# Kernel optimization log

Measured on AMD Instinct MI355X. Metric: run time of the kernel, lower is better.

The kernel has to match this reference:

```python
import jax, jax.numpy as jnp
import numpy as np
import math

D_MODEL = 1024
N_HEADS = 16
B, T = 4, 2048


def setup_inputs() -> dict:
    key = jax.random.key(0)
    ks = jax.random.split(key, 10)
    s = 1.0 / math.sqrt(D_MODEL)
    x = jax.random.normal(ks[0], (B, T, D_MODEL), dtype=jnp.float32)
    # causal mask, broadcastable over batch and heads; 0 -> masked
    mask = jnp.tril(jnp.ones((T, T), dtype=jnp.int32))[None, None, :, :]
    w_q = jax.random.normal(ks[1], (D_MODEL, D_MODEL), dtype=jnp.float32) * s
    b_q = jnp.zeros((D_MODEL,), dtype=jnp.float32)
    w_k = jax.random.normal(ks[2], (D_MODEL, D_MODEL), dtype=jnp.float32) * s
    b_k = jnp.zeros((D_MODEL,), dtype=jnp.float32)
    w_v = jax.random.normal(ks[3], (D_MODEL, D_MODEL), dtype=jnp.float32) * s
    b_v = jnp.zeros((D_MODEL,), dtype=jnp.float32)
    w_o = jax.random.normal(ks[4], (D_MODEL, D_MODEL), dtype=jnp.float32) * s
    b_o = jnp.zeros((D_MODEL,), dtype=jnp.float32)
    return {"x": x, "mask": mask, "w_q": w_q, "b_q": b_q, "w_k": w_k,
            "b_k": b_k, "w_v": w_v, "b_v": b_v, "w_o": w_o, "b_o": b_o}


def reference(x, mask, w_q, b_q, w_k, b_k, w_v, b_v, w_o, b_o):
    Bx, Tx, C = x.shape
    H = N_HEADS
    d_k = C // H
    def split_heads(y):  # [B,T,C] -> [B,H,T,d_k]
        return y.reshape(Bx, Tx, H, d_k).transpose(0, 2, 1, 3)
    Q = split_heads(x @ w_q + b_q)
    K = split_heads(x @ w_k + b_k)
    V = split_heads(x @ w_v + b_v)
    scores = jnp.einsum('bhqd,bhkd->bhqk', Q, K) / math.sqrt(d_k)
    scores = jnp.where(mask == 0, jnp.float32(-1e9), scores)
    attn = jax.nn.softmax(scores, axis=-1)
    out = jnp.einsum('bhqk,bhkd->bhqd', attn, V)
    out = out.transpose(0, 2, 1, 3).reshape(Bx, Tx, C)
    return out @ w_o + b_o
```

## Files before the change

### kernel.cpp

```cpp
#include <hip/hip_runtime.h>
#include <stdint.h>

#define D_MODEL 1024
#define NH      16
#define BB      4
#define TT      2048
#define MROWS   (BB * TT)

typedef __attribute__((ext_vector_type(8))) short bf16x8;
typedef __attribute__((ext_vector_type(4))) short bf16x4;
typedef __attribute__((ext_vector_type(4))) float f32x4;

__device__ __forceinline__ unsigned short f2bf(float f) {
    union { float f; unsigned int u; } v; v.f = f;
    unsigned int r = v.u + 0x7fffu + ((v.u >> 16) & 1u);
    return (unsigned short)(r >> 16);
}

__device__ __forceinline__ unsigned short f2bf_fast(float f) {
    union { float f; unsigned int u; } v; v.f = f;
    return (unsigned short)((v.u + 0x8000u) >> 16);
}

__device__ __forceinline__ f32x4 mfma_16x16x16_bf16(bf16x4 a, bf16x4 b, f32x4 c) {
    asm("v_mfma_f32_16x16x16_bf16 %0, %1, %2, %0" : "+v"(c) : "v"(a), "v"(b));
    return c;
}

__device__ __forceinline__ void gload_lds16(const unsigned short* g, unsigned short* l) {
    __builtin_amdgcn_global_load_lds(
        (const __attribute__((address_space(1))) void*)g,
        (__attribute__((address_space(3))) void*)l,
        16, 0, 0);
}

__global__ void convert_x_kernel(const float* __restrict__ x, unsigned short* __restrict__ xb) {
    int i = blockIdx.x * 256 + threadIdx.x;
    float4 v = ((const float4*)x)[i];
    ushort4 o;
    o.x = f2bf(v.x); o.y = f2bf(v.y); o.z = f2bf(v.z); o.w = f2bf(v.w);
    ((ushort4*)xb)[i] = o;
}

__global__ void transpose_w_kernel(const float* __restrict__ wq, const float* __restrict__ wk,
                                   const float* __restrict__ wv, const float* __restrict__ wo,
                                   unsigned short* tq, unsigned short* tk,
                                   unsigned short* tv, unsigned short* to_) {
    const float* src; unsigned short* dst;
    switch (blockIdx.z) {
        case 0:  src = wq; dst = tq; break;
        case 1:  src = wk; dst = tk; break;
        case 2:  src = wv; dst = tv; break;
        default: src = wo; dst = to_; break;
    }
    __shared__ float tile[32][33];
    int tx = threadIdx.x & 31, ty = threadIdx.x >> 5;
    int k0 = blockIdx.y * 32, n0 = blockIdx.x * 32;
    #pragma unroll
    for (int i = 0; i < 4; ++i)
        tile[ty + i * 8][tx] = src[(k0 + ty + i * 8) * D_MODEL + n0 + tx];
    __syncthreads();
    #pragma unroll
    for (int i = 0; i < 4; ++i)
        dst[(n0 + ty + i * 8) * D_MODEL + k0 + tx] = f2bf(tile[tx][ty + i * 8]);
}

__device__ __forceinline__ void gemm_mainloop(const unsigned short* __restrict__ A,
                                              const unsigned short* __restrict__ Bt,
                                              int m0, int n0,
                                              unsigned short* As, unsigned short* Bs,
                                              f32x4 acc[4][4]) {
    const int tid = threadIdx.x;
    const int lane = tid & 63, wave = tid >> 6;
    const int wm = (wave >> 1) * 64, wn = (wave & 1) * 64;
    const int l15 = lane & 15, quad = lane >> 4;
    const int rx7 = l15 & 7;
    const int srow = tid >> 3;
    const int scol = ((tid & 7) ^ (srow & 7)) * 8;
    const unsigned short* Ag = A + (size_t)(m0 + srow) * D_MODEL + scol;
    const unsigned short* Bg = Bt + (size_t)(n0 + srow) * D_MODEL + scol;
    unsigned short* AsW = As + wave * 512;
    unsigned short* BsW = Bs + wave * 512;
    for (int k0 = 0; k0 < D_MODEL; k0 += 64) {
        __syncthreads();
        #pragma unroll
        for (int p = 0; p < 4; ++p) {
            gload_lds16(Ag + k0 + (size_t)(32 * p) * D_MODEL, AsW + (32 * p) * 64);
            gload_lds16(Bg + k0 + (size_t)(32 * p) * D_MODEL, BsW + (32 * p) * 64);
        }
        __syncthreads();
        #pragma unroll
        for (int kk = 0; kk < 2; ++kk) {
            const int co = ((kk * 4 + quad) ^ rx7) * 8;
            bf16x8 af[4], bfr[4];
            #pragma unroll
            for (int mt = 0; mt < 4; ++mt)
                af[mt] = *(const bf16x8*)(As + (wm + mt * 16 + l15) * 64 + co);
            #pragma unroll
            for (int nt = 0; nt < 4; ++nt)
                bfr[nt] = *(const bf16x8*)(Bs + (wn + nt * 16 + l15) * 64 + co);
            #pragma unroll
            for (int mt = 0; mt < 4; ++mt)
                #pragma unroll
                for (int nt = 0; nt < 4; ++nt)
                    acc[mt][nt] = __builtin_amdgcn_mfma_f32_16x16x32_bf16(af[mt], bfr[nt], acc[mt][nt], 0, 0, 0);
        }
    }
}

__global__ __launch_bounds__(256, 2) void gemm_qkv_kernel(
        const unsigned short* __restrict__ Xb, const unsigned short* __restrict__ Wt,
        const float* __restrict__ bq, const float* __restrict__ bk, const float* __restrict__ bv,
        unsigned short* __restrict__ Qo, unsigned short* __restrict__ Ko,
        unsigned short* __restrict__ VTo) {
    __shared__ unsigned short S[18432];
    unsigned short* As = S;
    unsigned short* Bs = S + 8192;
    int m0 = blockIdx.y * 128, n0 = blockIdx.x * 128;
    f32x4 acc[4][4];
    #pragma unroll
    for (int mt = 0; mt < 4; ++mt)
        #pragma unroll
        for (int nt = 0; nt < 4; ++nt)
            acc[mt][nt] = (f32x4){0.f, 0.f, 0.f, 0.f};
    gemm_mainloop(Xb, Wt, m0, n0, As, Bs, acc);

    const int sel = n0 >> 10;
    const float* bias = (sel == 0) ? bq : (sel == 1) ? bk : bv;
    const float scale = (sel == 0) ? 0.125f * 1.44269504f : 1.f;
    const int tid = threadIdx.x, lane = tid & 63, wave = tid >> 6;
    const int wm = (wave >> 1) * 64, wn = (wave & 1) * 64, l15 = lane & 15, quad = lane >> 4;
    if (sel < 2) {
        unsigned short* Out = (sel == 0) ? Qo : Ko;
        __syncthreads();
        unsigned short* R = S + (wn >> 6) * 9216;
        #pragma unroll
        for (int nt = 0; nt < 4; ++nt) {
            int ln = nt * 16 + l15;
            int col = (n0 + wn + nt * 16 + l15) & 1023;
            float bv_ = bias[col];
            #pragma unroll
            for (int mt = 0; mt < 4; ++mt)
                #pragma unroll
                for (int r = 0; r < 4; ++r) {
                    int lm = wm + mt * 16 + quad * 4 + r;
                    R[lm * 72 + ln] = f2bf((acc[mt][nt][r] + bv_) * scale);
                }
        }
        __syncthreads();
        int hh = tid >> 7, t = tid & 127;
        int h0 = (n0 & 1023) >> 6;
        int b = m0 >> 11, tb = m0 & 2047;
        unsigned short* gp = Out + (size_t)((b * NH + h0 + hh) * TT + tb + t) * 64;
        const unsigned short* lp = S + hh * 9216 + t * 72;
        #pragma unroll
        for (int j = 0; j < 8; ++j)
            *(uint4*)(gp + j * 8) = *(const uint4*)(lp + j * 8);
    } else {
        #pragma unroll
        for (int nt = 0; nt < 4; ++nt) {
            int col = (n0 + wn + nt * 16 + l15) & 1023;
            float bv_ = bias[col];
            int h = col >> 6, dd = col & 63;
            #pragma unroll
            for (int mt = 0; mt < 4; ++mt) {
                int gm0 = m0 + wm + mt * 16 + quad * 4;
                int b = gm0 >> 11, t0 = gm0 & 2047;
                ushort4 o;
                o.x = f2bf(acc[mt][nt][0] + bv_);
                o.y = f2bf(acc[mt][nt][1] + bv_);
                o.z = f2bf(acc[mt][nt][2] + bv_);
                o.w = f2bf(acc[mt][nt][3] + bv_);
                *(ushort4*)&VTo[(((size_t)(b * NH + h) * 16 + (t0 >> 7)) * 64 + dd) * 128 + (t0 & 127)] = o;
            }
        }
    }
}

__global__ __launch_bounds__(256, 2) void gemm_out_kernel(
        const unsigned short* __restrict__ Ob, const unsigned short* __restrict__ Wto,
        const float* __restrict__ bo, float* __restrict__ out) {
    __shared__ unsigned short As[128 * 64], Bs[128 * 64];
    int m0 = blockIdx.y * 128, n0 = blockIdx.x * 128;
    f32x4 acc[4][4];
    #pragma unroll
    for (int mt = 0; mt < 4; ++mt)
        #pragma unroll
        for (int nt = 0; nt < 4; ++nt)
            acc[mt][nt] = (f32x4){0.f, 0.f, 0.f, 0.f};
    gemm_mainloop(Ob, Wto, m0, n0, As, Bs, acc);
    const int tid = threadIdx.x, lane = tid & 63, wave = tid >> 6;
    const int wm = (wave >> 1) * 64, wn = (wave & 1) * 64, l15 = lane & 15, quad = lane >> 4;
    #pragma unroll
    for (int nt = 0; nt < 4; ++nt) {
        int gn = n0 + wn + nt * 16 + l15;
        float bv_ = bo[gn];
        #pragma unroll
        for (int mt = 0; mt < 4; ++mt) {
            #pragma unroll
            for (int r = 0; r < 4; ++r) {
                int gm = m0 + wm + mt * 16 + quad * 4 + r;
                out[(size_t)gm * D_MODEL + gn] = acc[mt][nt][r] + bv_;
            }
        }
    }
}

__global__ __launch_bounds__(256, 4) void flash_kernel(
        const unsigned short* __restrict__ Q, const unsigned short* __restrict__ K,
        const unsigned short* __restrict__ VT, unsigned short* __restrict__ O) {
    __shared__ unsigned short S[16384];
    unsigned short* Kd = S;
    unsigned short* Vd = S + 8192;
    const int n = blockIdx.x;
    const int bh = n & 63;
    const int qt = 15 - (n >> 6);
    const int q0 = qt * 128;
    const int tid = threadIdx.x, lane = tid & 63, wave = tid >> 6;
    const int l15 = lane & 15, quad = lane >> 4;
    const int mbase = wave * 32;
    const unsigned short* Qb = Q + (size_t)bh * (TT * 64) + (size_t)q0 * 64;
    const unsigned short* Kb = K + (size_t)bh * (TT * 64);
    const unsigned short* Vtb = VT + (size_t)bh * (16 * 8192);

    int koff[2], voff[2];
    #pragma unroll
    for (int p = 0; p < 2; ++p) {
        int c = p * 256 + tid;
        int r = c >> 3, s = c & 7;
        koff[p] = r * 64 + ((s ^ (r & 7)) * 8);
        voff[p] = r * 128 + ((s ^ (r & 7)) * 8);
    }
    auto fire = [&](int kt, int buf) {
        const unsigned short* Ksrc = Kb + kt * 4096;
        const unsigned short* Vsrc = Vtb + (kt >> 1) * 8192 + (kt & 1) * 64;
        #pragma unroll
        for (int p = 0; p < 2; ++p) {
            gload_lds16(Ksrc + koff[p], Kd + buf * 4096 + (p * 256 + wave * 64) * 8);
            gload_lds16(Vsrc + voff[p], Vd + buf * 4096 + (p * 256 + wave * 64) * 8);
        }
    };

    bf16x8 qf[2][2];
    #pragma unroll
    for (int mt = 0; mt < 2; ++mt)
        #pragma unroll
        for (int kk = 0; kk < 2; ++kk)
            qf[mt][kk] = *(const bf16x8*)(Qb + (size_t)(mbase + mt * 16 + l15) * 64 + kk * 32 + quad * 8);

    float l_full[2] = {0.f, 0.f};
    f32x4 acc[2][4];
    #pragma unroll
    for (int mt = 0; mt < 2; ++mt)
        #pragma unroll
        for (int nt = 0; nt < 4; ++nt) acc[mt][nt] = (f32x4){0.f, 0.f, 0.f, 0.f};

    fire(0, 0);

    const int nkt = 2 * qt + 2;
    for (int kt = 0; kt < nkt; ++kt) {
        const int p = kt & 1;
        __syncthreads();
        if (kt + 1 < nkt) fire(kt + 1, p ^ 1);
        if (kt * 64 > q0 + mbase + 31) continue;
        const unsigned short* Ksl = Kd + p * 4096;
        const unsigned short* Vsl = Vd + p * 4096;

        #pragma unroll 1
        for (int s4 = 0; s4 < 2; ++s4) {
            f32x4 sf[2][2];
            #pragma unroll
            for (int mt = 0; mt < 2; ++mt)
                #pragma unroll
                for (int ntl = 0; ntl < 2; ++ntl) sf[mt][ntl] = (f32x4){0.f, 0.f, 0.f, 0.f};
            __builtin_amdgcn_s_setprio(1);
            #pragma unroll
            for (int kk = 0; kk < 2; ++kk)
                #pragma unroll
                for (int ntl = 0; ntl < 2; ++ntl) {
                    int row = s4 * 32 + ntl * 16 + l15;
                    bf16x8 kf = *(const bf16x8*)&Ksl[row * 64 + (((kk * 4 + quad) ^ (row & 7)) * 8)];
                    #pragma unroll
                    for (int mt = 0; mt < 2; ++mt)
                        sf[mt][ntl] = __builtin_amdgcn_mfma_f32_16x16x32_bf16(kf, qf[mt][kk], sf[mt][ntl], 0, 0, 0);
                }
            __builtin_amdgcn_s_setprio(0);
            if (kt >= 2 * qt) {
                const int kofs = (kt - 2 * qt) * 64;
                #pragma unroll
                for (int mt = 0; mt < 2; ++mt) {
                    int qi = mbase + mt * 16 + l15;
                    #pragma unroll
                    for (int ntl = 0; ntl < 2; ++ntl)
                        #pragma unroll
                        for (int r = 0; r < 4; ++r) {
                            int ki = kofs + s4 * 32 + ntl * 16 + quad * 4 + r;
                            if (ki > qi) sf[mt][ntl][r] = -1e30f;
                        }
                }
            }
            bf16x4 pa[2][2];
            #pragma unroll
            for (int mt = 0; mt < 2; ++mt)
                #pragma unroll
                for (int ntl = 0; ntl < 2; ++ntl) {
                    float p0 = __builtin_amdgcn_exp2f(sf[mt][ntl][0]);
                    float p1 = __builtin_amdgcn_exp2f(sf[mt][ntl][1]);
                    float p2 = __builtin_amdgcn_exp2f(sf[mt][ntl][2]);
                    float p3 = __builtin_amdgcn_exp2f(sf[mt][ntl][3]);
                    l_full[mt] += (p0 + p1) + (p2 + p3);
                    bf16x4 pk;
                    pk[0] = (short)f2bf_fast(p0);
                    pk[1] = (short)f2bf_fast(p1);
                    pk[2] = (short)f2bf_fast(p2);
                    pk[3] = (short)f2bf_fast(p3);
                    pa[mt][ntl] = pk;
                }
            __builtin_amdgcn_s_setprio(1);
            #pragma unroll
            for (int ntl = 0; ntl < 2; ++ntl) {
                #pragma unroll
                for (int ntv = 0; ntv < 4; ++ntv) {
                    int d = ntv * 16 + l15;
                    int cch = s4 * 4 + ntl * 2 + (quad >> 1);
                    bf16x4 vf = *(const bf16x4*)&Vsl[d * 64 + ((cch ^ (d & 7)) * 8) + (quad & 1) * 4];
                    #pragma unroll
                    for (int mt = 0; mt < 2; ++mt)
                        acc[mt][ntv] = mfma_16x16x16_bf16(pa[mt][ntl], vf, acc[mt][ntv]);
                }
            }
            __builtin_amdgcn_s_setprio(0);
        }
    }

    const int b = bh >> 4, h = bh & 15;
    float inv[2][4];
    #pragma unroll
    for (int mt = 0; mt < 2; ++mt) {
        float l = l_full[mt];
        l += __shfl_xor(l, 16);
        l += __shfl_xor(l, 32);
        #pragma unroll
        for (int r = 0; r < 4; ++r) {
            float lr = __shfl(l, quad * 4 + r);
            inv[mt][r] = __builtin_amdgcn_rcpf(lr);
        }
    }
    __syncthreads();
    unsigned short* Ost = S;
    #pragma unroll
    for (int mt = 0; mt < 2; ++mt)
        #pragma unroll
        for (int nt = 0; nt < 4; ++nt)
            #pragma unroll
            for (int r = 0; r < 4; ++r)
                Ost[(mbase + mt * 16 + quad * 4 + r) * 72 + nt * 16 + l15] =
                    f2bf(acc[mt][nt][r] * inv[mt][r]);
    __syncthreads();
    {
        int row = tid >> 1, seg = tid & 1;
        unsigned short* gp = O + (size_t)(b * TT + q0 + row) * D_MODEL + h * 64 + seg * 32;
        const unsigned short* lp = Ost + row * 72 + seg * 32;
        #pragma unroll
        for (int j = 0; j < 4; ++j)
            *(uint4*)(gp + j * 8) = *(const uint4*)(lp + j * 8);
    }
}

extern "C" void kernel_launch(void* const* d_in, const int* in_sizes, int n_in,
                              void* d_out, int out_size, void* d_ws, size_t ws_size,
                              hipStream_t stream) {
    const float* x  = (const float*)d_in[0];
    const float* wq = (const float*)d_in[2];
    const float* bq = (const float*)d_in[3];
    const float* wk = (const float*)d_in[4];
    const float* bk = (const float*)d_in[5];
    const float* wv = (const float*)d_in[6];
    const float* bv = (const float*)d_in[7];
    const float* wo = (const float*)d_in[8];
    const float* bo = (const float*)d_in[9];

    char* ws = (char*)d_ws;
    unsigned short* Xb  = (unsigned short*)ws;
    unsigned short* Wtq = (unsigned short*)(ws + (size_t)(16 << 20));
    unsigned short* Wtk = Wtq + (size_t)D_MODEL * D_MODEL;
    unsigned short* Wtv = Wtk + (size_t)D_MODEL * D_MODEL;
    unsigned short* Wto = Wtv + (size_t)D_MODEL * D_MODEL;
    unsigned short* Qb  = Wto + (size_t)D_MODEL * D_MODEL;
    unsigned short* Kb  = Qb + (size_t)MROWS * D_MODEL;
    unsigned short* VTb = Kb + (size_t)MROWS * D_MODEL;
    unsigned short* Ob  = Xb;

    convert_x_kernel<<<(MROWS * D_MODEL) / (256 * 4), 256, 0, stream>>>(x, Xb);
    transpose_w_kernel<<<dim3(32, 32, 4), 256, 0, stream>>>(wq, wk, wv, wo, Wtq, Wtk, Wtv, Wto);
    gemm_qkv_kernel<<<dim3(3 * D_MODEL / 128, MROWS / 128), 256, 0, stream>>>(
        Xb, Wtq, bq, bk, bv, Qb, Kb, VTb);
    flash_kernel<<<dim3(16 * 64), 256, 0, stream>>>(Qb, Kb, VTb, Ob);
    gemm_out_kernel<<<dim3(D_MODEL / 128, MROWS / 128), 256, 0, stream>>>(Ob, Wto, bo, (float*)d_out);
}
```

Baseline: 264.4 us.

## Merge x conversion into weight transpose kernel and batch QK over both sub-tiles

Folds the fp32-to-bf16 conversion of x into the weight transpose kernel as an extra grid slice, removing one kernel launch. In the flash kernel, the two 32-key sub-tiles are now unrolled so that both QK^T products are issued before masking and softmax. This is meant to give the scheduler more independent MFMA work and overlap exp with matrix ops. The cost is higher register pressure, which could lower occupancy.

```diff
diff --git a/kernel.cpp b/kernel.cpp
--- a/kernel.cpp
+++ b/kernel.cpp
@@ -34,18 +34,23 @@
         16, 0, 0);
 }
 
-__global__ void convert_x_kernel(const float* __restrict__ x, unsigned short* __restrict__ xb) {
-    int i = blockIdx.x * 256 + threadIdx.x;
-    float4 v = ((const float4*)x)[i];
-    ushort4 o;
-    o.x = f2bf(v.x); o.y = f2bf(v.y); o.z = f2bf(v.z); o.w = f2bf(v.w);
-    ((ushort4*)xb)[i] = o;
-}
-
-__global__ void transpose_w_kernel(const float* __restrict__ wq, const float* __restrict__ wk,
-                                   const float* __restrict__ wv, const float* __restrict__ wo,
-                                   unsigned short* tq, unsigned short* tk,
-                                   unsigned short* tv, unsigned short* to_) {
+__global__ void prep_kernel(const float* __restrict__ x, unsigned short* __restrict__ xb,
+                            const float* __restrict__ wq, const float* __restrict__ wk,
+                            const float* __restrict__ wv, const float* __restrict__ wo,
+                            unsigned short* tq, unsigned short* tk,
+                            unsigned short* tv, unsigned short* to_) {
+    if (blockIdx.z == 4) {
+        int base = (blockIdx.y * 32 + blockIdx.x) * 2048 + threadIdx.x;
+        #pragma unroll
+        for (int j = 0; j < 8; ++j) {
+            int i = base + j * 256;
+            float4 v = ((const float4*)x)[i];
+            ushort4 o;
+            o.x = f2bf(v.x); o.y = f2bf(v.y); o.z = f2bf(v.z); o.w = f2bf(v.w);
+            ((ushort4*)xb)[i] = o;
+        }
+        return;
+    }
     const float* src; unsigned short* dst;
     switch (blockIdx.z) {
         case 0:  src = wq; dst = tq; break;
@@ -266,14 +271,16 @@
         const unsigned short* Ksl = Kd + p * 4096;
         const unsigned short* Vsl = Vd + p * 4096;
 
-        #pragma unroll 1
-        for (int s4 = 0; s4 < 2; ++s4) {
-            f32x4 sf[2][2];
+        f32x4 sf[2][2][2];
+        #pragma unroll
+        for (int s4 = 0; s4 < 2; ++s4)
             #pragma unroll
             for (int mt = 0; mt < 2; ++mt)
                 #pragma unroll
-                for (int ntl = 0; ntl < 2; ++ntl) sf[mt][ntl] = (f32x4){0.f, 0.f, 0.f, 0.f};
-            __builtin_amdgcn_s_setprio(1);
+                for (int ntl = 0; ntl < 2; ++ntl) sf[s4][mt][ntl] = (f32x4){0.f, 0.f, 0.f, 0.f};
+        __builtin_amdgcn_s_setprio(1);
+        #pragma unroll
+        for (int s4 = 0; s4 < 2; ++s4)
             #pragma unroll
             for (int kk = 0; kk < 2; ++kk)
                 #pragma unroll
@@ -282,11 +289,13 @@
                     bf16x8 kf = *(const bf16x8*)&Ksl[row * 64 + (((kk * 4 + quad) ^ (row & 7)) * 8)];
                     #pragma unroll
                     for (int mt = 0; mt < 2; ++mt)
-                        sf[mt][ntl] = __builtin_amdgcn_mfma_f32_16x16x32_bf16(kf, qf[mt][kk], sf[mt][ntl], 0, 0, 0);
+                        sf[s4][mt][ntl] = __builtin_amdgcn_mfma_f32_16x16x32_bf16(kf, qf[mt][kk], sf[s4][mt][ntl], 0, 0, 0);
                 }
-            __builtin_amdgcn_s_setprio(0);
-            if (kt >= 2 * qt) {
-                const int kofs = (kt - 2 * qt) * 64;
+        __builtin_amdgcn_s_setprio(0);
+        if (kt >= 2 * qt) {
+            const int kofs = (kt - 2 * qt) * 64;
+            #pragma unroll
+            for (int s4 = 0; s4 < 2; ++s4)
                 #pragma unroll
                 for (int mt = 0; mt < 2; ++mt) {
                     int qi = mbase + mt * 16 + l15;
@@ -295,26 +304,28 @@
                         #pragma unroll
                         for (int r = 0; r < 4; ++r) {
                             int ki = kofs + s4 * 32 + ntl * 16 + quad * 4 + r;
-                            if (ki > qi) sf[mt][ntl][r] = -1e30f;
+                            if (ki > qi) sf[s4][mt][ntl][r] = -1e30f;
                         }
                 }
-            }
-            bf16x4 pa[2][2];
+        }
+        bf16x4 pa[2][2][2];
+        #pragma unroll
+        for (int s4 = 0; s4 < 2; ++s4) {
             #pragma unroll
             for (int mt = 0; mt < 2; ++mt)
                 #pragma unroll
                 for (int ntl = 0; ntl < 2; ++ntl) {
-                    float p0 = __builtin_amdgcn_exp2f(sf[mt][ntl][0]);
-                    float p1 = __builtin_amdgcn_exp2f(sf[mt][ntl][1]);
-                    float p2 = __builtin_amdgcn_exp2f(sf[mt][ntl][2]);
-                    float p3 = __builtin_amdgcn_exp2f(sf[mt][ntl][3]);
+                    float p0 = __builtin_amdgcn_exp2f(sf[s4][mt][ntl][0]);
+                    float p1 = __builtin_amdgcn_exp2f(sf[s4][mt][ntl][1]);
+                    float p2 = __builtin_amdgcn_exp2f(sf[s4][mt][ntl][2]);
+                    float p3 = __builtin_amdgcn_exp2f(sf[s4][mt][ntl][3]);
                     l_full[mt] += (p0 + p1) + (p2 + p3);
                     bf16x4 pk;
                     pk[0] = (short)f2bf_fast(p0);
                     pk[1] = (short)f2bf_fast(p1);
                     pk[2] = (short)f2bf_fast(p2);
                     pk[3] = (short)f2bf_fast(p3);
-                    pa[mt][ntl] = pk;
+                    pa[s4][mt][ntl] = pk;
                 }
             __builtin_amdgcn_s_setprio(1);
             #pragma unroll
@@ -326,7 +337,7 @@
                     bf16x4 vf = *(const bf16x4*)&Vsl[d * 64 + ((cch ^ (d & 7)) * 8) + (quad & 1) * 4];
                     #pragma unroll
                     for (int mt = 0; mt < 2; ++mt)
-                        acc[mt][ntv] = mfma_16x16x16_bf16(pa[mt][ntl], vf, acc[mt][ntv]);
+                        acc[mt][ntv] = mfma_16x16x16_bf16(pa[s4][mt][ntl], vf, acc[mt][ntv]);
                 }
             }
             __builtin_amdgcn_s_setprio(0);
@@ -391,8 +402,7 @@
     unsigned short* VTb = Kb + (size_t)MROWS * D_MODEL;
     unsigned short* Ob  = Xb;
 
-    convert_x_kernel<<<(MROWS * D_MODEL) / (256 * 4), 256, 0, stream>>>(x, Xb);
-    transpose_w_kernel<<<dim3(32, 32, 4), 256, 0, stream>>>(wq, wk, wv, wo, Wtq, Wtk, Wtv, Wto);
+    prep_kernel<<<dim3(32, 32, 5), 256, 0, stream>>>(x, Xb, wq, wk, wv, wo, Wtq, Wtk, Wtv, Wto);
     gemm_qkv_kernel<<<dim3(3 * D_MODEL / 128, MROWS / 128), 256, 0, stream>>>(
         Xb, Wtq, bq, bk, bv, Qb, Kb, VTb);
     flash_kernel<<<dim3(16 * 64), 256, 0, stream>>>(Qb, Kb, VTb, Ob);
```

After: 261.9 us. No clear change (-1.0%).
